# Kernel tuning notes

Measured on AMD Instinct MI355X. Metric: run time of the kernel, lower is better.

Reference implementation:

```python
import jax, jax.numpy as jnp
import numpy as np

EPS = 1e-12  # matches torch F.normalize eps


def _l2norm(t):
    n = jnp.linalg.norm(t, axis=-1, keepdims=True)
    return t / jnp.maximum(n, EPS)


def setup_inputs() -> dict:
    key = jax.random.key(0)
    ks = jax.random.split(key, 10)
    B, N, C = 2, 2048, 384
    nH, hd = 12, 32
    inp = {
        "x": jax.random.normal(ks[0], (B, N, C), jnp.float32),
        "q_w": jax.random.normal(ks[1], (C, C), jnp.float32) * 0.02,
        "q_b": jax.random.normal(ks[2], (C,), jnp.float32) * 0.02,
        "kv_w": jax.random.normal(ks[3], (2 * C, C), jnp.float32) * 0.02,
        "kv_b": jax.random.normal(ks[4], (2 * C,), jnp.float32) * 0.02,
        "query_embedding": jax.random.normal(ks[5], (nH, 1, hd), jnp.float32) * 0.02,
        # init of temperature in torch: log(exp(1/0.24) - 1)
        "temperature": jnp.full((nH, 1, 1), float(np.log(np.exp(1.0 / 0.24) - 1.0)), jnp.float32),
        "pos_bias": jax.random.normal(ks[7], (nH, N), jnp.float32) * 0.0004,
        "proj_w": jax.random.normal(ks[8], (C, C), jnp.float32) * 0.02,
        "proj_b": jax.random.normal(ks[9], (C,), jnp.float32) * 0.02,
        "D": 8, "H": 16, "W": 16,
    }
    return inp


def reference(x, q_w, q_b, kv_w, kv_b, query_embedding, temperature, pos_bias, proj_w, proj_b, D, H, W):
    B, N, C = x.shape
    nH, hd = query_embedding.shape[0], query_embedding.shape[2]
    assert N == D * H * W
    # q projection -> [B, nH, N, hd], cosine-normalized
    q = (x @ q_w.T + q_b).reshape(B, N, nH, hd).transpose(0, 2, 1, 3)
    q = _l2norm(q)
    # additive query embedding, softplus temperature, seq-length (log N) scale
    scale = jax.nn.softplus(temperature) * jnp.float32(np.log(N))  # [nH,1,1]
    q = (q + query_embedding[None]) * scale[None]
    # kv projection
    kv = x @ kv_w.T + kv_b  # [B, N, 2C]
    k, v = kv[..., :C], kv[..., C:]
    k = _l2norm(k.reshape(B, N, nH, hd).transpose(0, 2, 1, 3))
    v = v.reshape(B, N, nH, hd).transpose(0, 2, 1, 3)
    # scores with per-head learned positional bias over keys
    attn = jnp.einsum("bhqd,bhkd->bhqk", q, k) + pos_bias[None, :, None, :]
    attn = jax.nn.softmax(attn, axis=-1)
    out = jnp.einsum("bhqk,bhkd->bhqd", attn, v)
    out = out.transpose(0, 2, 1, 3).reshape(B, N, C)
    return out @ proj_w.T + proj_b
```

## Files before the change

### kernel.cpp

```cpp
#include <hip/hip_runtime.h>

#define LOG2E 1.4426950408889634f

typedef __bf16 bf16x8 __attribute__((ext_vector_type(8)));
typedef short s16x4 __attribute__((ext_vector_type(4)));
typedef float f32x4 __attribute__((ext_vector_type(4)));

#define BB 2
#define NN 2048
#define CC 384
#define NH 12
#define HD 32
#define MROWS (BB * NN)

__device__ __forceinline__ unsigned short f2bf(float f) {
  __bf16 h = (__bf16)f;
  return __builtin_bit_cast(unsigned short, h);
}

__device__ __forceinline__ bf16x8 ldg_bf8(const unsigned short* p) {
  uint4 v = *reinterpret_cast<const uint4*>(p);
  return __builtin_bit_cast(bf16x8, v);
}

__device__ __forceinline__ float fexp2(float x) {
#if __has_builtin(__builtin_amdgcn_exp2f)
  return __builtin_amdgcn_exp2f(x);
#else
  return exp2f(x);
#endif
}

__device__ __forceinline__ s16x4 pack_bf4(float a, float b, float c, float d) {
#if __has_builtin(__builtin_amdgcn_cvt_pk_bf16_f32)
  auto lo = __builtin_amdgcn_cvt_pk_bf16_f32(a, b);
  auto hi = __builtin_amdgcn_cvt_pk_bf16_f32(c, d);
  uint2 u = {__builtin_bit_cast(unsigned int, lo),
             __builtin_bit_cast(unsigned int, hi)};
  return __builtin_bit_cast(s16x4, u);
#else
  s16x4 r = {(short)f2bf(a), (short)f2bf(b), (short)f2bf(c), (short)f2bf(d)};
  return r;
#endif
}

typedef __attribute__((address_space(1))) const void gas_void;
typedef __attribute__((address_space(3))) void las_void;
__device__ __forceinline__ void gload_lds16(const void* g, void* l) {
  __builtin_amdgcn_global_load_lds((gas_void*)(unsigned long long)g,
                                   (las_void*)(unsigned long long)l, 16, 0, 0);
}

__device__ __forceinline__ f32x4 mfma32(bf16x8 a, bf16x8 b, f32x4 c) {
  return __builtin_amdgcn_mfma_f32_16x16x32_bf16(a, b, c, 0, 0, 0);
}

__device__ __forceinline__ f32x4 mfma16(s16x4 a, s16x4 b, f32x4 c) {
#if defined(__HIP_DEVICE_COMPILE__)
#if __has_builtin(__builtin_amdgcn_mfma_f32_16x16x16bf16_1k)
  return __builtin_amdgcn_mfma_f32_16x16x16bf16_1k(a, b, c, 0, 0, 0);
#else
  asm volatile("v_mfma_f32_16x16x16_bf16 %0, %1, %2, %0"
               : "+v"(c) : "v"(a), "v"(b));
  return c;
#endif
#else
  return c;
#endif
}

__global__ __launch_bounds__(256) void prep_kernel(
    const float* __restrict__ x, const float* __restrict__ q_w,
    const float* __restrict__ kv_w, const float* __restrict__ proj_w,
    const float* __restrict__ pos_bias, unsigned short* __restrict__ xb,
    unsigned short* __restrict__ qwb, unsigned short* __restrict__ kvwb,
    unsigned short* __restrict__ pwb, float* __restrict__ bias2) {
  int i = blockIdx.x * 256 + threadIdx.x;
  if (i < 1572864) { xb[i] = f2bf(x[i]); return; }
  i -= 1572864;
  if (i < 147456) { qwb[i] = f2bf(q_w[i]); return; }
  i -= 147456;
  if (i < 294912) { kvwb[i] = f2bf(kv_w[i]); return; }
  i -= 294912;
  if (i < 147456) { pwb[i] = f2bf(proj_w[i]); return; }
  i -= 147456;
  bias2[i] = pos_bias[i] * LOG2E;
}

__global__ __launch_bounds__(256, 4) void gemm_qkv_norm_kernel(
    const unsigned short* __restrict__ xb, const unsigned short* __restrict__ qwb,
    const unsigned short* __restrict__ kvwb, const float* __restrict__ q_b,
    const float* __restrict__ kv_b, const float* __restrict__ qe,
    const float* __restrict__ temperature, unsigned short* __restrict__ Qs,
    unsigned short* __restrict__ Kn, unsigned short* __restrict__ VT) {
  __shared__ alignas(16) char smem[2][20480];
  int wave = threadIdx.x >> 6, lane = threadIdx.x & 63;
  int c = lane & 15, quad = lane >> 4;
  int h = blockIdx.y;
  int m0b = blockIdx.x * 64;
  int cid = wave * 64 + lane;

  auto stage = [&](int buf, int kk) {
    char* base = smem[buf];
#pragma unroll
    for (int j = 0; j < 2; ++j) {
      int chunk = j * 256 + cid;
      int row = chunk >> 3, e = chunk & 7;
      gload_lds16(xb + (long)(m0b + row) * CC + kk + e * 8,
                  base + j * 4096 + wave * 1024);
    }
#pragma unroll
    for (int j = 0; j < 3; ++j) {
      int chunk = j * 256 + cid;
      int row = chunk >> 3, e = chunk & 7;
      const unsigned short* src;
      if (row < 32)      src = qwb + (long)(h * 32 + row) * CC;
      else if (row < 64) src = kvwb + (long)(h * 32 + (row - 32)) * CC;
      else               src = kvwb + (long)(CC + h * 32 + (row - 64)) * CC;
      gload_lds16(src + kk + e * 8, base + 8192 + j * 4096 + wave * 1024);
    }
  };

  f32x4 acc[6] = {};
  auto compute = [&](int buf) {
    const char* base = smem[buf];
#pragma unroll
    for (int kh = 0; kh < 2; ++kh) {
      bf16x8 a = *(const bf16x8*)(base + (wave * 16 + c) * 128 + kh * 64 + quad * 16);
#pragma unroll
      for (int t = 0; t < 6; ++t) {
        bf16x8 b = *(const bf16x8*)(base + 8192 + (t * 16 + c) * 128 + kh * 64 + quad * 16);
        acc[t] = mfma32(a, b, acc[t]);
      }
    }
  };

  stage(0, 0);
#pragma unroll 1
  for (int s = 0; s < 6; ++s) {
    __syncthreads();
    if (s < 5) stage((s + 1) & 1, (s + 1) * 64);
    compute(s & 1);
  }

  int m0 = m0b + wave * 16;
  float qb0 = q_b[h * 32 + c], qb1 = q_b[h * 32 + 16 + c];
  float kb0 = kv_b[h * 32 + c], kb1 = kv_b[h * 32 + 16 + c];
  float vb0 = kv_b[CC + h * 32 + c], vb1 = kv_b[CC + h * 32 + 16 + c];
  float qe0 = qe[h * HD + c], qe1 = qe[h * HD + 16 + c];
  float sc = log1pf(expf(temperature[h])) * 11.0f;
  int b = m0 >> 11;
  int nb = (m0 & 2047) + quad * 4;
  int pair = b * NH + h;
  unsigned short* qsb = Qs + ((long)pair * NN + nb) * HD;
  unsigned short* knb = Kn + ((long)pair * NN + nb) * HD;
  ushort4 vp0, vp1;
#pragma unroll
  for (int r = 0; r < 4; ++r) {
    float q0 = acc[0][r] + qb0, q1 = acc[1][r] + qb1;
    float k0 = acc[2][r] + kb0, k1 = acc[3][r] + kb1;
    float v0 = acc[4][r] + vb0, v1 = acc[5][r] + vb1;
    float qs = q0 * q0 + q1 * q1, ks = k0 * k0 + k1 * k1;
#pragma unroll
    for (int off = 8; off; off >>= 1) {
      qs += __shfl_xor(qs, off);
      ks += __shfl_xor(ks, off);
    }
    float qi = 1.0f / fmaxf(sqrtf(qs), 1e-12f);
    float ki = 1.0f / fmaxf(sqrtf(ks), 1e-12f);
    qsb[r * HD + c] = f2bf((q0 * qi + qe0) * sc);
    qsb[r * HD + 16 + c] = f2bf((q1 * qi + qe1) * sc);
    knb[r * HD + c] = f2bf(k0 * ki);
    knb[r * HD + 16 + c] = f2bf(k1 * ki);
    ((unsigned short*)&vp0)[r] = f2bf(v0);
    ((unsigned short*)&vp1)[r] = f2bf(v1);
  }
  *reinterpret_cast<ushort4*>(VT + ((long)pair * HD + c) * NN + nb) = vp0;
  *reinterpret_cast<ushort4*>(VT + ((long)pair * HD + 16 + c) * NN + nb) = vp1;
}

__global__ __launch_bounds__(256, 4) void attn_kernel(
    const unsigned short* __restrict__ Qs, const unsigned short* __restrict__ Kn,
    const unsigned short* __restrict__ VT, const float* __restrict__ bias2,
    unsigned short* __restrict__ ao) {
  __shared__ alignas(16) char smem[2][16384];
  __shared__ alignas(16) char biasl[8192];
  int wave = threadIdx.x >> 6, lane = threadIdx.x & 63;
  int c = lane & 15, quad = lane >> 4;
  int id = blockIdx.x;
  int xcd = id & 7, rr = id >> 3;
  int pair = (rr >> 5) * 8 + xcd;
  int qt = rr & 31;
  int h = pair % NH, b = pair / NH;
  const unsigned short* Qp = Qs + (long)pair * NN * HD;
  const char* Kg0 = (const char*)(Kn + (long)pair * NN * HD);
  const char* Vg0 = (const char*)(VT + (long)pair * HD * NN);
  const char* bp = (const char*)(bias2 + h * NN);
  int q0 = qt * 64 + wave * 16;
  bf16x8 qf = ldg_bf8(Qp + (long)(q0 + c) * HD + quad * 8);
  f32x4 o0 = {}, o1 = {};
  float rs = 0.f;

  const int koff = (c * 4 + quad) * 16;

  auto stage = [&](int buf, int i) {
    char* tb = smem[buf];
    long krow0 = (long)i * 128;
    const char* Kg = Kg0 + krow0 * (HD * 2);
    const char* Vg = Vg0 + krow0 * 2;
#pragma unroll
    for (int j = 0; j < 2; ++j) {
      int ck = wave * 2 + j;
      gload_lds16(Kg + ck * 1024 + koff, tb + ck * 1024);
      int chunk = ck * 64 + lane;
      int d = chunk >> 4, e = chunk & 15;
      int es = e ^ (d & 15);
      gload_lds16(Vg + (long)d * (NN * 2) + es * 16, tb + 8192 + ck * 1024);
    }
  };

  auto compute = [&](int buf, int i) {
    const char* kb = smem[buf] + lane * 16;
    const char* vb = smem[buf] + 8192;
    const char* bl = biasl + i * 512 + quad * 16;
#pragma unroll
    for (int t8 = 0; t8 < 8; ++t8) {
      bf16x8 kf = *(const bf16x8*)(kb + t8 * 1024);
      f32x4 bbv = *(const f32x4*)(bl + t8 * 64);
      f32x4 s = mfma32(kf, qf, bbv);
      float p0 = fexp2(s[0]);
      float p1 = fexp2(s[1]);
      float p2 = fexp2(s[2]);
      float p3 = fexp2(s[3]);
      rs += (p0 + p1) + (p2 + p3);
      s16x4 pf = pack_bf4(p0, p1, p2, p3);
      int vsw = (((t8 * 2 + (quad >> 1)) ^ c) * 16) + (quad & 1) * 8;
      s16x4 vlo = *(const s16x4*)(vb + c * 256 + vsw);
      s16x4 vhi = *(const s16x4*)(vb + (c + 16) * 256 + vsw);
      o0 = mfma16(vlo, pf, o0);
      o1 = mfma16(vhi, pf, o1);
    }
  };

#pragma unroll
  for (int j = 0; j < 2; ++j)
    gload_lds16(bp + j * 4096 + wave * 1024 + lane * 16,
                biasl + j * 4096 + wave * 1024);
  stage(0, 0);
#pragma unroll 1
  for (int i = 0; i < 16; ++i) {
    __syncthreads();
    if (i < 15) stage((i + 1) & 1, i + 1);
    compute(i & 1, i);
  }

  rs += __shfl_xor(rs, 16);
  rs += __shfl_xor(rs, 32);
  float inv = 1.0f / rs;
  unsigned short* op = ao + (long)(b * NN + q0 + c) * CC + h * HD + quad * 4;
  ushort4 s0, s1;
#pragma unroll
  for (int r = 0; r < 4; ++r) {
    ((unsigned short*)&s0)[r] = f2bf(o0[r] * inv);
    ((unsigned short*)&s1)[r] = f2bf(o1[r] * inv);
  }
  *reinterpret_cast<ushort4*>(op) = s0;
  *reinterpret_cast<ushort4*>(op + 16) = s1;
}

__global__ __launch_bounds__(256, 4) void proj_kernel(
    const unsigned short* __restrict__ ab, const unsigned short* __restrict__ pwb,
    const float* __restrict__ proj_b, float* __restrict__ out) {
  __shared__ alignas(16) char smem[2][16384];
  int wave = threadIdx.x >> 6, lane = threadIdx.x & 63;
  int c = lane & 15, quad = lane >> 4;
  int m0b = blockIdx.x * 64;
  int n0 = blockIdx.y * 64;
  int cid = wave * 64 + lane;

  auto stage = [&](int buf, int kk) {
    char* base = smem[buf];
#pragma unroll
    for (int j = 0; j < 2; ++j) {
      int chunk = j * 256 + cid;
      int row = chunk >> 3, e = chunk & 7;
      gload_lds16(ab + (long)(m0b + row) * CC + kk + e * 8,
                  base + j * 4096 + wave * 1024);
      gload_lds16(pwb + (long)(n0 + row) * CC + kk + e * 8,
                  base + 8192 + j * 4096 + wave * 1024);
    }
  };

  f32x4 acc[4] = {};
  auto compute = [&](int buf) {
    const char* base = smem[buf];
#pragma unroll
    for (int kh = 0; kh < 2; ++kh) {
      bf16x8 a = *(const bf16x8*)(base + (wave * 16 + c) * 128 + kh * 64 + quad * 16);
#pragma unroll
      for (int t = 0; t < 4; ++t) {
        bf16x8 b = *(const bf16x8*)(base + 8192 + (t * 16 + c) * 128 + kh * 64 + quad * 16);
        acc[t] = mfma32(a, b, acc[t]);
      }
    }
  };

  stage(0, 0);
#pragma unroll 1
  for (int s = 0; s < 6; ++s) {
    __syncthreads();
    if (s < 5) stage((s + 1) & 1, (s + 1) * 64);
    compute(s & 1);
  }

  int m0 = m0b + wave * 16;
#pragma unroll
  for (int t = 0; t < 4; ++t) {
    int o = n0 + t * 16 + c;
    float bv = proj_b[o];
#pragma unroll
    for (int r = 0; r < 4; ++r) {
      out[(long)(m0 + quad * 4 + r) * CC + o] = acc[t][r] + bv;
    }
  }
}

extern "C" void kernel_launch(void* const* d_in, const int* in_sizes, int n_in,
                              void* d_out, int out_size, void* d_ws, size_t ws_size,
                              hipStream_t stream) {
  const float* x = (const float*)d_in[0];
  const float* q_w = (const float*)d_in[1];
  const float* q_b = (const float*)d_in[2];
  const float* kv_w = (const float*)d_in[3];
  const float* kv_b = (const float*)d_in[4];
  const float* qe = (const float*)d_in[5];
  const float* temp = (const float*)d_in[6];
  const float* pos_bias = (const float*)d_in[7];
  const float* proj_w = (const float*)d_in[8];
  const float* proj_b = (const float*)d_in[9];
  float* out = (float*)d_out;

  char* ws = (char*)d_ws;
  unsigned short* xb = (unsigned short*)(ws + 0);
  unsigned short* qwb = (unsigned short*)(ws + 3145728);
  unsigned short* kvwb = (unsigned short*)(ws + 3440640);
  unsigned short* pwb = (unsigned short*)(ws + 4030464);
  unsigned short* Qs = (unsigned short*)(ws + 4325376);
  unsigned short* Kn = (unsigned short*)(ws + 7471104);
  unsigned short* VT = (unsigned short*)(ws + 10616832);
  unsigned short* ao = (unsigned short*)(ws + 13762560);
  float* bias2 = (float*)(ws + 16908288);

  prep_kernel<<<8544, 256, 0, stream>>>(x, q_w, kv_w, proj_w, pos_bias, xb, qwb,
                                        kvwb, pwb, bias2);
  gemm_qkv_norm_kernel<<<dim3(64, NH), 256, 0, stream>>>(xb, qwb, kvwb, q_b, kv_b,
                                                         qe, temp, Qs, Kn, VT);
  attn_kernel<<<768, 256, 0, stream>>>(Qs, Kn, VT, bias2, ao);
  proj_kernel<<<dim3(64, 6), 256, 0, stream>>>(ao, pwb, proj_b, out);
}
```

Baseline: 132.9 us.

## Vectorize prep casts, XOR-swizzle GEMM LDS tiles, halve proj N tile

The prep kernel now converts eight floats per thread with float4 loads and 16-byte stores, which cuts the launch from 8544 blocks to 1068. The QKV and projection GEMMs load their global data into LDS with an XOR swizzle on the 16-byte chunk index, and the reads use the matching swizzle to avoid LDS bank conflicts. The projection kernel's N tile shrinks from 64 to 32 columns, doubling its grid to 768 blocks for better CU occupancy at the cost of more A-tile reloads. The prep kernel relies on pack_bf4, which must exist in the unseen part of the file.

```diff
diff --git a/kernel.cpp b/kernel.cpp
--- a/kernel.cpp
+++ b/kernel.cpp
@@ -75,16 +75,30 @@
     const float* __restrict__ pos_bias, unsigned short* __restrict__ xb,
     unsigned short* __restrict__ qwb, unsigned short* __restrict__ kvwb,
     unsigned short* __restrict__ pwb, float* __restrict__ bias2) {
-  int i = blockIdx.x * 256 + threadIdx.x;
-  if (i < 1572864) { xb[i] = f2bf(x[i]); return; }
+  long i = (long)(blockIdx.x * 256 + threadIdx.x) * 8;
+  auto cast8 = [&](const float* s, unsigned short* d, long off) {
+    float4 a = *reinterpret_cast<const float4*>(s + off);
+    float4 b = *reinterpret_cast<const float4*>(s + off + 4);
+    s16x4 lo = pack_bf4(a.x, a.y, a.z, a.w);
+    s16x4 hi = pack_bf4(b.x, b.y, b.z, b.w);
+    uint2 l = __builtin_bit_cast(uint2, lo), h = __builtin_bit_cast(uint2, hi);
+    uint4 o = {l.x, l.y, h.x, h.y};
+    *reinterpret_cast<uint4*>(d + off) = o;
+  };
+  if (i < 1572864) { cast8(x, xb, i); return; }
   i -= 1572864;
-  if (i < 147456) { qwb[i] = f2bf(q_w[i]); return; }
+  if (i < 147456) { cast8(q_w, qwb, i); return; }
   i -= 147456;
-  if (i < 294912) { kvwb[i] = f2bf(kv_w[i]); return; }
+  if (i < 294912) { cast8(kv_w, kvwb, i); return; }
   i -= 294912;
-  if (i < 147456) { pwb[i] = f2bf(proj_w[i]); return; }
+  if (i < 147456) { cast8(proj_w, pwb, i); return; }
   i -= 147456;
-  bias2[i] = pos_bias[i] * LOG2E;
+  float4 a = *reinterpret_cast<const float4*>(pos_bias + i);
+  float4 b = *reinterpret_cast<const float4*>(pos_bias + i + 4);
+  a.x *= LOG2E; a.y *= LOG2E; a.z *= LOG2E; a.w *= LOG2E;
+  b.x *= LOG2E; b.y *= LOG2E; b.z *= LOG2E; b.w *= LOG2E;
+  *reinterpret_cast<float4*>(bias2 + i) = a;
+  *reinterpret_cast<float4*>(bias2 + i + 4) = b;
 }
 
 __global__ __launch_bounds__(256, 4) void gemm_qkv_norm_kernel(
@@ -106,7 +120,7 @@
     for (int j = 0; j < 2; ++j) {
       int chunk = j * 256 + cid;
       int row = chunk >> 3, e = chunk & 7;
-      gload_lds16(xb + (long)(m0b + row) * CC + kk + e * 8,
+      gload_lds16(xb + (long)(m0b + row) * CC + kk + (e ^ (row & 7)) * 8,
                   base + j * 4096 + wave * 1024);
     }
 #pragma unroll
@@ -117,7 +131,8 @@
       if (row < 32)      src = qwb + (long)(h * 32 + row) * CC;
       else if (row < 64) src = kvwb + (long)(h * 32 + (row - 32)) * CC;
       else               src = kvwb + (long)(CC + h * 32 + (row - 64)) * CC;
-      gload_lds16(src + kk + e * 8, base + 8192 + j * 4096 + wave * 1024);
+      gload_lds16(src + kk + (e ^ (row & 7)) * 8,
+                  base + 8192 + j * 4096 + wave * 1024);
     }
   };
 
@@ -126,10 +141,11 @@
     const char* base = smem[buf];
 #pragma unroll
     for (int kh = 0; kh < 2; ++kh) {
-      bf16x8 a = *(const bf16x8*)(base + (wave * 16 + c) * 128 + kh * 64 + quad * 16);
+      int sa = ((kh * 4 + quad) ^ (c & 7)) * 16;
+      bf16x8 a = *(const bf16x8*)(base + (wave * 16 + c) * 128 + sa);
 #pragma unroll
       for (int t = 0; t < 6; ++t) {
-        bf16x8 b = *(const bf16x8*)(base + 8192 + (t * 16 + c) * 128 + kh * 64 + quad * 16);
+        bf16x8 b = *(const bf16x8*)(base + 8192 + (t * 16 + c) * 128 + sa);
         acc[t] = mfma32(a, b, acc[t]);
       }
     }
@@ -271,11 +287,11 @@
 __global__ __launch_bounds__(256, 4) void proj_kernel(
     const unsigned short* __restrict__ ab, const unsigned short* __restrict__ pwb,
     const float* __restrict__ proj_b, float* __restrict__ out) {
-  __shared__ alignas(16) char smem[2][16384];
+  __shared__ alignas(16) char smem[2][12288];
   int wave = threadIdx.x >> 6, lane = threadIdx.x & 63;
   int c = lane & 15, quad = lane >> 4;
   int m0b = blockIdx.x * 64;
-  int n0 = blockIdx.y * 64;
+  int n0 = blockIdx.y * 32;
   int cid = wave * 64 + lane;
 
   auto stage = [&](int buf, int kk) {
@@ -284,22 +300,26 @@
     for (int j = 0; j < 2; ++j) {
       int chunk = j * 256 + cid;
       int row = chunk >> 3, e = chunk & 7;
-      gload_lds16(ab + (long)(m0b + row) * CC + kk + e * 8,
+      gload_lds16(ab + (long)(m0b + row) * CC + kk + (e ^ (row & 7)) * 8,
                   base + j * 4096 + wave * 1024);
-      gload_lds16(pwb + (long)(n0 + row) * CC + kk + e * 8,
-                  base + 8192 + j * 4096 + wave * 1024);
-    }
-  };
-
-  f32x4 acc[4] = {};
+    }
+    {
+      int row = cid >> 3, e = cid & 7;
+      gload_lds16(pwb + (long)(n0 + row) * CC + kk + (e ^ (row & 7)) * 8,
+                  base + 8192 + wave * 1024);
+    }
+  };
+
+  f32x4 acc[2] = {};
   auto compute = [&](int buf) {
     const char* base = smem[buf];
 #pragma unroll
     for (int kh = 0; kh < 2; ++kh) {
-      bf16x8 a = *(const bf16x8*)(base + (wave * 16 + c) * 128 + kh * 64 + quad * 16);
-#pragma unroll
-      for (int t = 0; t < 4; ++t) {
-        bf16x8 b = *(const bf16x8*)(base + 8192 + (t * 16 + c) * 128 + kh * 64 + quad * 16);
+      int sa = ((kh * 4 + quad) ^ (c & 7)) * 16;
+      bf16x8 a = *(const bf16x8*)(base + (wave * 16 + c) * 128 + sa);
+#pragma unroll
+      for (int t = 0; t < 2; ++t) {
+        bf16x8 b = *(const bf16x8*)(base + 8192 + (t * 16 + c) * 128 + sa);
         acc[t] = mfma32(a, b, acc[t]);
       }
     }
@@ -315,7 +335,7 @@
 
   int m0 = m0b + wave * 16;
 #pragma unroll
-  for (int t = 0; t < 4; ++t) {
+  for (int t = 0; t < 2; ++t) {
     int o = n0 + t * 16 + c;
     float bv = proj_b[o];
 #pragma unroll
@@ -351,10 +371,10 @@
   unsigned short* ao = (unsigned short*)(ws + 13762560);
   float* bias2 = (float*)(ws + 16908288);
 
-  prep_kernel<<<8544, 256, 0, stream>>>(x, q_w, kv_w, proj_w, pos_bias, xb, qwb,
+  prep_kernel<<<1068, 256, 0, stream>>>(x, q_w, kv_w, proj_w, pos_bias, xb, qwb,
                                         kvwb, pwb, bias2);
   gemm_qkv_norm_kernel<<<dim3(64, NH), 256, 0, stream>>>(xb, qwb, kvwb, q_b, kv_b,
                                                          qe, temp, Qs, Kn, VT);
   attn_kernel<<<768, 256, 0, stream>>>(Qs, Kn, VT, bias2, ao);
-  proj_kernel<<<dim3(64, 6), 256, 0, stream>>>(ao, pwb, proj_b, out);
-}
+  proj_kernel<<<dim3(64, 12), 256, 0, stream>>>(ao, pwb, proj_b, out);
+}
```

New measurement: 124.9 us. 1.06x faster.
